# Kernel tuning notes

Measured on AMD Instinct MI355X. Metric: run time of the kernel, lower is better.

## Reference

```python
import jax, jax.numpy as jnp
import numpy as np

H = 512
IN = 512
T = 1024
B = 64


def setup_inputs() -> dict:
    key = jax.random.key(0)
    ks = jax.random.split(key, 17)
    s_in = 1.0 / np.sqrt(IN)
    s_h = 1.0 / np.sqrt(H)
    inp = {"x": jax.random.normal(ks[0], (T, B, IN), dtype=jnp.float32)}
    names = [("Wxf", "bxf", True), ("Whf", "bhf", False),
             ("Wxi", "bxi", True), ("Whi", "bhi", False),
             ("Wxo", "bxo", True), ("Who", "bho", False),
             ("Wxg", "bxg", True), ("Whg", "bhg", False)]
    i = 1
    for wn, bn, is_x in names:
        fan = IN if is_x else H
        s = s_in if is_x else s_h
        inp[wn] = jax.random.uniform(ks[i], (H, fan), minval=-s, maxval=s, dtype=jnp.float32)
        inp[bn] = jax.random.uniform(ks[i + 1], (H,), minval=-s, maxval=s, dtype=jnp.float32)
        i += 2
    return inp


def _lstm(x, Wxf, bxf, Whf, bhf, Wxi, bxi, Whi, bhi,
          Wxo, bxo, Who, bho, Wxg, bxg, Whg, bhg):
    # Stack 8 gate linears into 2 GEMMs (same math, gate order f,i,o,g)
    Wx = jnp.concatenate([Wxf, Wxi, Wxo, Wxg], axis=0)   # (4H, IN)
    Wh = jnp.concatenate([Whf, Whi, Who, Whg], axis=0)   # (4H, H)
    b = jnp.concatenate([bxf, bxi, bxo, bxg]) + jnp.concatenate([bhf, bhi, bho, bhg])
    # Precompute input projections for all timesteps: (T, B, 4H)
    xp = jnp.einsum('tbi,gi->tbg', x, Wx) + b
    h0 = jnp.zeros((x.shape[1], Whf.shape[0]), dtype=x.dtype)
    c0 = jnp.zeros_like(h0)

    def step(carry, xpt):
        h, c = carry
        z = xpt + h @ Wh.T                       # (B, 4H)
        f, i, o, g = jnp.split(z, 4, axis=-1)
        f = jax.nn.sigmoid(f)
        i = jax.nn.sigmoid(i)
        o = jax.nn.sigmoid(o)
        c = f * c + i * jnp.tanh(g)
        h = o * jnp.tanh(c)
        return (h, c), h

    (h, c), h_seq = jax.lax.scan(step, (h0, c0), xp)
    return h_seq, h[None], c[None]


def reference(x, Wxf, bxf, Whf, bhf, Wxi, bxi, Whi, bhi,
              Wxo, bxo, Who, bho, Wxg, bxg, Whg, bhg):
    return _lstm(x, Wxf, bxf, Whf, bhf, Wxi, bxi, Whi, bhi,
                 Wxo, bxo, Who, bho, Wxg, bxg, Whg, bhg)
```

## Files before the change

### kernel.cpp

```cpp
#include <hip/hip_runtime.h>


#define TT 1024
#define BB 64
#define DD 512
#define NWG 32
#define HSEQ ((size_t)TT * BB * DD)

typedef _Float16 half8 __attribute__((ext_vector_type(8)));
typedef float f32x4 __attribute__((ext_vector_type(4)));

__device__ __forceinline__ float sigm(float v) { return 1.0f / (1.0f + __expf(-v)); }
__device__ __forceinline__ float tanh_fast(float v) { return 2.0f / (1.0f + __expf(-2.0f * v)) - 1.0f; }

#define CVT8(DST, LO, HI) do { \
    DST[0] = (_Float16)LO[0]; DST[1] = (_Float16)LO[1]; \
    DST[2] = (_Float16)LO[2]; DST[3] = (_Float16)LO[3]; \
    DST[4] = (_Float16)HI[0]; DST[5] = (_Float16)HI[1]; \
    DST[6] = (_Float16)HI[2]; DST[7] = (_Float16)HI[3]; } while (0)

#define MFMA16(A, B, C) __builtin_amdgcn_mfma_f32_16x16x32_f16(A, B, C, 0, 0, 0)

__global__ __launch_bounds__(512, 2) void lstm_persist(
    const float* __restrict__ x,
    const float* __restrict__ Wxf, const float* __restrict__ Whf,
    const float* __restrict__ Wxi, const float* __restrict__ Whi,
    const float* __restrict__ Wxo, const float* __restrict__ Who,
    const float* __restrict__ Wxg, const float* __restrict__ Whg,
    const float* __restrict__ bxf, const float* __restrict__ bhf,
    const float* __restrict__ bxi, const float* __restrict__ bhi,
    const float* __restrict__ bxo, const float* __restrict__ bho,
    const float* __restrict__ bxg, const float* __restrict__ bhg,
    float* __restrict__ out, int* __restrict__ flags)
{
    const int wg   = blockIdx.x;
    const int grp  = wg >> 4;
    const int w    = wg & 15;
    const int tid  = threadIdx.x;
    const int wid  = tid >> 6;
    const int lane = tid & 63;
    const int quad = lane >> 4;
    const int l16  = lane & 15;
    const int g    = wid & 3;
    const bool is_h = wid >= 4;
    const int sid  = tid & 255;

    __shared__ _Float16 xlds[32][520];
    __shared__ _Float16 hlds[32][520];
    __shared__ float zx[4][32][33];
    __shared__ float zh[4][32][33];
    __shared__ float c_lds[32][33];
    __shared__ float bias_lds[4][32];

    {
        const int e = tid * 2, b = e >> 5, u = e & 31;
        c_lds[b][u] = 0.0f; c_lds[b][u + 1] = 0.0f;
    }
    if (tid < 128) {
        const int gg = tid >> 5, uu = tid & 31;
        const float* bx = (gg == 0) ? bxf : (gg == 1) ? bxi : (gg == 2) ? bxo : bxg;
        const float* bh = (gg == 0) ? bhf : (gg == 1) ? bhi : (gg == 2) ? bho : bhg;
        bias_lds[gg][uu] = bx[w * 32 + uu] + bh[w * 32 + uu];
    }

    const float* Ws = !is_h
        ? ((g == 0) ? Wxf : (g == 1) ? Wxi : (g == 2) ? Wxo : Wxg)
        : ((g == 0) ? Whf : (g == 1) ? Whi : (g == 2) ? Who : Whg);
    half8 wfrag[2][16];
#pragma unroll
    for (int n = 0; n < 2; ++n)
#pragma unroll
        for (int kc = 0; kc < 16; ++kc) {
            const float* p = Ws + (size_t)(w * 32 + n * 16 + l16) * DD + kc * 32 + quad * 8;
            f32x4 lo = *(const f32x4*)p;
            f32x4 hi = *(const f32x4*)(p + 4);
            half8 f; CVT8(f, lo, hi);
            wfrag[n][kc] = f;
        }

    const float* xbase = x   + (size_t)grp * 32 * DD;
    const float* obase = out + (size_t)grp * 32 * DD;
    const int*   fb    = flags + grp * 16 + (lane & 15);

    __syncthreads();

    for (int t = 0; t < TT; ++t) {
        if (!is_h) {
            const float* src = xbase + (size_t)t * BB * DD;
#pragma unroll 4
            for (int i = 0; i < 8; ++i) {
                const int flat = i * 2048 + sid * 8;
                const int r = flat >> 9, c = flat & 511;
                const float* p = src + (size_t)r * DD + c;
                f32x4 lo = *(const f32x4*)p;
                f32x4 hi = *(const f32x4*)(p + 4);
                half8 v; CVT8(v, lo, hi);
                *(half8*)&xlds[r][c] = v;
            }
        } else if (t > 0) {
            for (;;) {
                int f;
                asm volatile("global_load_dword %0, %1, off sc0 sc1\n\ts_waitcnt vmcnt(0)"
                             : "=&v"(f) : "v"(fb) : "memory");
                if (__all(f >= t)) break;
                __builtin_amdgcn_s_sleep(1);
            }
            const float* src = obase + (size_t)(t - 1) * BB * DD;
#pragma unroll 4
            for (int i = 0; i < 8; ++i) {
                const int flat = i * 2048 + sid * 8;
                const int r = flat >> 9, c = flat & 511;
                const float* p = src + (size_t)r * DD + c;
                f32x4 lo = *(const f32x4*)p;
                f32x4 hi = *(const f32x4*)(p + 4);
                half8 v; CVT8(v, lo, hi);
                *(half8*)&hlds[r][c] = v;
            }
        }
        __syncthreads();

        f32x4 acc00 = {0.f, 0.f, 0.f, 0.f}, acc01 = {0.f, 0.f, 0.f, 0.f};
        f32x4 acc10 = {0.f, 0.f, 0.f, 0.f}, acc11 = {0.f, 0.f, 0.f, 0.f};
        if (!is_h || t > 0) {
            const _Float16 (*alds)[520] = is_h ? hlds : xlds;
#pragma unroll
            for (int kc = 0; kc < 16; ++kc) {
                half8 a0 = *(const half8*)&alds[l16][kc * 32 + quad * 8];
                half8 a1 = *(const half8*)&alds[16 + l16][kc * 32 + quad * 8];
                acc00 = MFMA16(a0, wfrag[0][kc], acc00);
                acc01 = MFMA16(a0, wfrag[1][kc], acc01);
                acc10 = MFMA16(a1, wfrag[0][kc], acc10);
                acc11 = MFMA16(a1, wfrag[1][kc], acc11);
            }
        }
        {
            float (*zb)[33] = is_h ? zh[g] : zx[g];
#pragma unroll
            for (int i = 0; i < 4; ++i) {
                zb[quad * 4 + i][l16]           = acc00[i];
                zb[quad * 4 + i][16 + l16]      = acc01[i];
                zb[16 + quad * 4 + i][l16]      = acc10[i];
                zb[16 + quad * 4 + i][16 + l16] = acc11[i];
            }
        }
        __syncthreads();

        {
            const int e = tid * 2, b = e >> 5, u = e & 31;
            float h2[2];
#pragma unroll
            for (int k = 0; k < 2; ++k) {
                const int uu = u + k;
                float zf = bias_lds[0][uu] + zx[0][b][uu] + zh[0][b][uu];
                float zi = bias_lds[1][uu] + zx[1][b][uu] + zh[1][b][uu];
                float zo = bias_lds[2][uu] + zx[2][b][uu] + zh[2][b][uu];
                float zg = bias_lds[3][uu] + zx[3][b][uu] + zh[3][b][uu];
                float c  = sigm(zf) * c_lds[b][uu] + sigm(zi) * tanh_fast(zg);
                c_lds[b][uu] = c;
                h2[k] = sigm(zo) * tanh_fast(c);
            }
            float* hp = out + (size_t)t * BB * DD + (size_t)(grp * 32 + b) * DD + w * 32 + u;
            uint2 hv;
            hv.x = __builtin_bit_cast(unsigned, h2[0]);
            hv.y = __builtin_bit_cast(unsigned, h2[1]);
            asm volatile("global_store_dwordx2 %0, %1, off sc0 sc1"
                         :: "v"(hp), "v"(hv) : "memory");
            if (t == TT - 1) {
                float* fp2 = out + HSEQ + (size_t)(grp * 32 + b) * DD + w * 32 + u;
                fp2[0] = h2[0]; fp2[1] = h2[1];
            }
        }
        asm volatile("s_waitcnt vmcnt(0)" ::: "memory");
        __syncthreads();
        if (tid == 0) {
            int val = t + 1;
            int* fp = flags + grp * 16 + w;
            asm volatile("global_store_dword %0, %1, off sc0 sc1"
                         :: "v"(fp), "v"(val) : "memory");
        }
    }

    {
        const int e = tid * 2, b = e >> 5, u = e & 31;
        float* cp = out + HSEQ + (size_t)BB * DD + (size_t)(grp * 32 + b) * DD + w * 32 + u;
        cp[0] = c_lds[b][u];
        cp[1] = c_lds[b][u + 1];
    }
}

extern "C" void kernel_launch(void* const* d_in, const int* in_sizes, int n_in,
                              void* d_out, int out_size, void* d_ws, size_t ws_size,
                              hipStream_t stream) {
    const float* x   = (const float*)d_in[0];
    const float* Wxf = (const float*)d_in[1];  const float* bxf = (const float*)d_in[2];
    const float* Whf = (const float*)d_in[3];  const float* bhf = (const float*)d_in[4];
    const float* Wxi = (const float*)d_in[5];  const float* bxi = (const float*)d_in[6];
    const float* Whi = (const float*)d_in[7];  const float* bhi = (const float*)d_in[8];
    const float* Wxo = (const float*)d_in[9];  const float* bxo = (const float*)d_in[10];
    const float* Who = (const float*)d_in[11]; const float* bho = (const float*)d_in[12];
    const float* Wxg = (const float*)d_in[13]; const float* bxg = (const float*)d_in[14];
    const float* Whg = (const float*)d_in[15]; const float* bhg = (const float*)d_in[16];
    float* out = (float*)d_out;
    int* flags = (int*)d_ws;

    hipMemsetAsync(d_ws, 0, (size_t)NWG * sizeof(int), stream);

    void* args[] = { &x,
                     &Wxf, &Whf, &Wxi, &Whi, &Wxo, &Who, &Wxg, &Whg,
                     &bxf, &bhf, &bxi, &bhi, &bxo, &bho, &bxg, &bhg,
                     &out, &flags };
    hipLaunchCooperativeKernel((const void*)lstm_persist,
                               dim3(NWG), dim3(512), args, 0, stream);
}
```

Baseline: 5.223 ms.

## Exchange hidden state via double-buffered fp16 workspace instead of fp32 output

Each workgroup now writes its new h values as packed fp16 into a double-buffered exchange area in the workspace. The h-loading waves read that buffer with cache-bypassing loads, which halves the bytes crossing the inter-workgroup dependency and removes the fp32-to-fp16 conversion on the critical path. The main fp32 output store becomes an ordinary store, the LDS row padding goes from 33 to 34, and the h waves raise their scheduling priority during load and MFMA. The cost is an extra store per step and reliance on workspace size and double-buffer correctness.

```diff
diff --git a/kernel.cpp b/kernel.cpp
--- a/kernel.cpp
+++ b/kernel.cpp
@@ -6,9 +6,11 @@
 #define DD 512
 #define NWG 32
 #define HSEQ ((size_t)TT * BB * DD)
+#define EXOFF 4096
 
 typedef _Float16 half8 __attribute__((ext_vector_type(8)));
 typedef float f32x4 __attribute__((ext_vector_type(4)));
+typedef float f32x2 __attribute__((ext_vector_type(2)));
 
 __device__ __forceinline__ float sigm(float v) { return 1.0f / (1.0f + __expf(-v)); }
 __device__ __forceinline__ float tanh_fast(float v) { return 2.0f / (1.0f + __expf(-2.0f * v)) - 1.0f; }
@@ -20,6 +22,34 @@
     DST[6] = (_Float16)HI[2]; DST[7] = (_Float16)HI[3]; } while (0)
 
 #define MFMA16(A, B, C) __builtin_amdgcn_mfma_f32_16x16x32_f16(A, B, C, 0, 0, 0)
+
+__device__ __forceinline__ void load_ex8(const char* base, f32x4 r[8]) {
+    const char* p0 = base;
+    const char* p1 = base + 4096;
+    const char* p2 = base + 8192;
+    const char* p3 = base + 12288;
+    const char* p4 = base + 16384;
+    const char* p5 = base + 20480;
+    const char* p6 = base + 24576;
+    const char* p7 = base + 28672;
+    f32x4 a0, a1, a2, a3, a4, a5, a6, a7;
+    asm volatile(
+        "global_load_dwordx4 %0, %8, off sc0 sc1\n\t"
+        "global_load_dwordx4 %1, %9, off sc0 sc1\n\t"
+        "global_load_dwordx4 %2, %10, off sc0 sc1\n\t"
+        "global_load_dwordx4 %3, %11, off sc0 sc1\n\t"
+        "global_load_dwordx4 %4, %12, off sc0 sc1\n\t"
+        "global_load_dwordx4 %5, %13, off sc0 sc1\n\t"
+        "global_load_dwordx4 %6, %14, off sc0 sc1\n\t"
+        "global_load_dwordx4 %7, %15, off sc0 sc1\n\t"
+        "s_waitcnt vmcnt(0)"
+        : "=&v"(a0), "=&v"(a1), "=&v"(a2), "=&v"(a3),
+          "=&v"(a4), "=&v"(a5), "=&v"(a6), "=&v"(a7)
+        : "v"(p0), "v"(p1), "v"(p2), "v"(p3), "v"(p4), "v"(p5), "v"(p6), "v"(p7)
+        : "memory");
+    r[0] = a0; r[1] = a1; r[2] = a2; r[3] = a3;
+    r[4] = a4; r[5] = a5; r[6] = a6; r[7] = a7;
+}
 
 __global__ __launch_bounds__(512, 2) void lstm_persist(
     const float* __restrict__ x,
@@ -31,7 +61,7 @@
     const float* __restrict__ bxi, const float* __restrict__ bhi,
     const float* __restrict__ bxo, const float* __restrict__ bho,
     const float* __restrict__ bxg, const float* __restrict__ bhg,
-    float* __restrict__ out, int* __restrict__ flags)
+    float* __restrict__ out, int* __restrict__ flags, char* __restrict__ ex)
 {
     const int wg   = blockIdx.x;
     const int grp  = wg >> 4;
@@ -47,9 +77,9 @@
 
     __shared__ _Float16 xlds[32][520];
     __shared__ _Float16 hlds[32][520];
-    __shared__ float zx[4][32][33];
-    __shared__ float zh[4][32][33];
-    __shared__ float c_lds[32][33];
+    __shared__ float zx[4][32][34];
+    __shared__ float zh[4][32][34];
+    __shared__ float c_lds[32][34];
     __shared__ float bias_lds[4][32];
 
     {
@@ -78,13 +108,15 @@
             wfrag[n][kc] = f;
         }
 
-    const float* xbase = x   + (size_t)grp * 32 * DD;
-    const float* obase = out + (size_t)grp * 32 * DD;
+    const float* xbase = x + (size_t)grp * 32 * DD;
     const int*   fb    = flags + grp * 16 + (lane & 15);
+    char* exg = ex + ((size_t)grp << 15);
 
     __syncthreads();
 
     for (int t = 0; t < TT; ++t) {
+        if (is_h) __builtin_amdgcn_s_setprio(1);
+
         if (!is_h) {
             const float* src = xbase + (size_t)t * BB * DD;
 #pragma unroll 4
@@ -105,16 +137,15 @@
                 if (__all(f >= t)) break;
                 __builtin_amdgcn_s_sleep(1);
             }
-            const float* src = obase + (size_t)(t - 1) * BB * DD;
-#pragma unroll 4
+            const char* src = exg + (((t & 1) ^ 1) << 16) + sid * 16;
+            f32x4 rr[8];
+            load_ex8(src, rr);
+#pragma unroll
             for (int i = 0; i < 8; ++i) {
                 const int flat = i * 2048 + sid * 8;
                 const int r = flat >> 9, c = flat & 511;
-                const float* p = src + (size_t)r * DD + c;
-                f32x4 lo = *(const f32x4*)p;
-                f32x4 hi = *(const f32x4*)(p + 4);
-                half8 v; CVT8(v, lo, hi);
-                *(half8*)&hlds[r][c] = v;
+                union { f32x4 f; half8 h; } u; u.f = rr[i];
+                *(half8*)&hlds[r][c] = u.h;
             }
         }
         __syncthreads();
@@ -134,7 +165,7 @@
             }
         }
         {
-            float (*zb)[33] = is_h ? zh[g] : zx[g];
+            float (*zb)[34] = is_h ? zh[g] : zx[g];
 #pragma unroll
             for (int i = 0; i < 4; ++i) {
                 zb[quad * 4 + i][l16]           = acc00[i];
@@ -143,6 +174,7 @@
                 zb[16 + quad * 4 + i][16 + l16] = acc11[i];
             }
         }
+        if (is_h) __builtin_amdgcn_s_setprio(0);
         __syncthreads();
 
         {
@@ -160,15 +192,17 @@
                 h2[k] = sigm(zo) * tanh_fast(c);
             }
             float* hp = out + (size_t)t * BB * DD + (size_t)(grp * 32 + b) * DD + w * 32 + u;
-            uint2 hv;
-            hv.x = __builtin_bit_cast(unsigned, h2[0]);
-            hv.y = __builtin_bit_cast(unsigned, h2[1]);
-            asm volatile("global_store_dwordx2 %0, %1, off sc0 sc1"
-                         :: "v"(hp), "v"(hv) : "memory");
+            *(f32x2*)hp = (f32x2){h2[0], h2[1]};
             if (t == TT - 1) {
                 float* fp2 = out + HSEQ + (size_t)(grp * 32 + b) * DD + w * 32 + u;
                 fp2[0] = h2[0]; fp2[1] = h2[1];
             }
+            union { _Float16 h[2]; unsigned u32; } pk;
+            pk.h[0] = (_Float16)h2[0]; pk.h[1] = (_Float16)h2[1];
+            char* dst = exg + ((t & 1) << 16)
+                      + ((size_t)b * 512 + (w * 32 + u)) * 2;
+            asm volatile("global_store_dword %0, %1, off sc0 sc1"
+                         :: "v"(dst), "v"(pk.u32) : "memory");
         }
         asm volatile("s_waitcnt vmcnt(0)" ::: "memory");
         __syncthreads();
@@ -202,13 +236,14 @@
     const float* Whg = (const float*)d_in[15]; const float* bhg = (const float*)d_in[16];
     float* out = (float*)d_out;
     int* flags = (int*)d_ws;
+    char* ex = (char*)d_ws + EXOFF;
 
     hipMemsetAsync(d_ws, 0, (size_t)NWG * sizeof(int), stream);
 
     void* args[] = { &x,
                      &Wxf, &Whf, &Wxi, &Whi, &Wxo, &Who, &Wxg, &Whg,
                      &bxf, &bhf, &bxi, &bhi, &bxo, &bho, &bxg, &bhg,
-                     &out, &flags };
+                     &out, &flags, &ex };
     hipLaunchCooperativeKernel((const void*)lstm_persist,
                                dim3(NWG), dim3(512), args, 0, stream);
 }
```

Result: faster. 5.028 ms (-3.7%).
